# Optimization experiments

Hardware: AMD Instinct MI355X
Metric: run time of the kernel (lower is better)

Reference implementation:

```python
import jax, jax.numpy as jnp
import numpy as np

B, T, D, N = 8, 2048, 1024, 256


def setup_inputs() -> dict:
    key = jax.random.key(0)
    ks = jax.random.split(key, 6)
    sD = 1.0 / np.sqrt(D)
    sN = 1.0 / np.sqrt(N)
    return {
        "x": jax.random.normal(ks[0], (B, T, D), dtype=jnp.float32),
        "Wa": jax.random.normal(ks[1], (D, N), dtype=jnp.float32) * sD,
        "ba": jnp.zeros((N,), jnp.float32),
        "Wb": jax.random.normal(ks[2], (D, N), dtype=jnp.float32) * sD,
        "bb": jnp.zeros((N,), jnp.float32),
        "Wc": jax.random.normal(ks[3], (D, N), dtype=jnp.float32) * sD,
        "bc": jnp.zeros((N,), jnp.float32),
        "Wd": jax.random.normal(ks[4], (D, D), dtype=jnp.float32) * sD,
        "bd": jnp.zeros((D,), jnp.float32),
        "Wy": jax.random.normal(ks[5], (N, D), dtype=jnp.float32) * sN,
        "by": jnp.zeros((D,), jnp.float32),
    }


def reference(x, Wa, ba, Wb, bb, Wc, bc, Wd, bd, Wy, by):
    # Precompute all input-dependent gates/projections in batched GEMMs.
    a = jax.nn.sigmoid(jnp.einsum("btd,dn->btn", x, Wa) + ba)  # (B,T,N)
    b = jnp.einsum("btd,dn->btn", x, Wb) + bb                   # (B,T,N)
    c = jnp.tanh(jnp.einsum("btd,dn->btn", x, Wc) + bc)          # (B,T,N)
    d = jnp.einsum("btd,de->bte", x, Wd) + bd                    # (B,T,D)

    # Sequential linear-gated recurrence: s_t = a_t*s_{t-1} + (1-a_t)*b_t
    def step(s, abc):
        at, bt, ct = abc
        s = at * s + (1.0 - at) * bt
        return s, ct * s

    aT = jnp.swapaxes(a, 0, 1)  # (T,B,N)
    bT = jnp.swapaxes(b, 0, 1)
    cT = jnp.swapaxes(c, 0, 1)
    s0 = jnp.zeros((x.shape[0], Wa.shape[1]), x.dtype)
    _, csT = jax.lax.scan(step, s0, (aT, bT, cT))  # (T,B,N)
    cs = jnp.swapaxes(csT, 0, 1)                    # (B,T,N)

    # Output projection applied once over the full sequence.
    y = jnp.einsum("btn,nd->btd", cs, Wy) + by + d  # (B,T,D)
    return y
```

## Files before the change

### kernel.cpp

```cpp
#include <hip/hip_runtime.h>
#include <hip/hip_bf16.h>

typedef unsigned short u16;
typedef __attribute__((ext_vector_type(8))) short bf16x8;
typedef __attribute__((ext_vector_type(4))) float f32x4;

#define AS1 __attribute__((address_space(1)))
#define AS3 __attribute__((address_space(3)))

#define Bx 8
#define Tt 2048
#define Dd 1024
#define Nn 256
#define Mm (Bx*Tt)
#define CHAINS (Bx*Nn)
#define NCH 32
#define TC 64
#define NCOMB 1792

#define WS_NEED 105644032u

#define CVT_BLOCKS (Mm*Dd/8/256)
#define PACK_BLOCKS (32*32*5)

__device__ __forceinline__ u16 f2bf(float f) {
  union { float f; unsigned u; } v; v.f = f;
  unsigned u = v.u;
  u += 0x7fffu + ((u >> 16) & 1u);
  return (u16)(u >> 16);
}

__device__ __forceinline__ float bf2f(u16 h) {
  union { unsigned u; float f; } v; v.u = ((unsigned)h) << 16;
  return v.f;
}

__device__ __forceinline__ void gload_lds16(const void* g, void* l) {
  __builtin_amdgcn_global_load_lds((AS1 void*)(g), (AS3 void*)(l), 16, 0, 0);
}

__global__ void prep_kernel(const float* __restrict__ x, u16* __restrict__ xb,
                            const float* __restrict__ Wa, const float* __restrict__ Wb,
                            const float* __restrict__ Wc, const float* __restrict__ Wd,
                            const float* __restrict__ Wy,
                            u16* __restrict__ Wcomb, u16* __restrict__ Wyt) {
  const int bid = blockIdx.x;
  if (bid < CVT_BLOCKS) {
    int i = bid * blockDim.x + threadIdx.x;
    #pragma unroll
    for (int j = 0; j < 2; ++j) {
      float4 v = ((const float4*)x)[2*i + j];
      unsigned lo = (unsigned)f2bf(v.x) | ((unsigned)f2bf(v.y) << 16);
      unsigned hi = (unsigned)f2bf(v.z) | ((unsigned)f2bf(v.w) << 16);
      ((uint2*)xb)[2*i + j] = make_uint2(lo, hi);
    }
    return;
  }
  __shared__ float tile[32][33];
  const int pid = bid - CVT_BLOCKS;
  const int z = pid >> 10;
  const int rem = pid & 1023;
  const int bx = rem & 31, by = rem >> 5;
  const float* src; u16* dst; int R, C, dld;
  if (z < 3)       { src = (z==0?Wa:(z==1?Wb:Wc)); dst = Wcomb + (size_t)z*256*1024; R=1024; C=256;  dld=1024; }
  else if (z == 3) { src = Wd; dst = Wcomb + (size_t)768*1024; R=1024; C=1024; dld=1024; }
  else             { src = Wy; dst = Wyt; R=256;  C=1024; dld=256;  }
  int c0 = bx * 32, r0 = by * 32;
  if (c0 >= C || r0 >= R) return;
  int tx = threadIdx.x & 31, ty = threadIdx.x >> 5;
  #pragma unroll
  for (int i = 0; i < 32; i += 8)
    tile[ty + i][tx] = src[(size_t)(r0 + ty + i)*C + (c0 + tx)];
  __syncthreads();
  #pragma unroll
  for (int i = 0; i < 32; i += 8) {
    int c = c0 + ty + i, r = r0 + tx;
    dst[(size_t)c*dld + r] = f2bf(tile[tx][ty + i]);
  }
}

template<int EPI>
__global__ __launch_bounds__(512, 4) void gemm_bt_kernel(
    const u16* __restrict__ A, const u16* __restrict__ Bt, int K, int gx,
    u16* __restrict__ outA, float* __restrict__ outO, u16* __restrict__ dtmp,
    const float* __restrict__ b0, const float* __restrict__ b1,
    const float* __restrict__ b2, const float* __restrict__ b3) {
  __shared__ u16 ldsA[256*64];
  __shared__ u16 ldsB[128*64];
  const int tid = threadIdx.x;
  const int lane = tid & 63, wid = tid >> 6;
  const int wm = wid >> 1, wn = wid & 1;

  const int h = blockIdx.x;
  const int id = (h & 7) * (gridDim.x >> 3) + (h >> 3);
  const int mt = id / gx, nt = id % gx;
  const int m0 = mt * 256, n0 = nt * 128;

  f32x4 acc[4][4] = {};

  const int rl  = tid >> 3;
  const int ssl = (tid & 7) ^ (rl & 7);

  auto stage = [&](int k0) {
    #pragma unroll
    for (int u = 0; u < 4; ++u)
      gload_lds16(A + (size_t)(m0 + u*64 + rl)*K + k0 + ssl*8,
                  ldsA + u*4096 + tid*8);
    #pragma unroll
    for (int u = 0; u < 2; ++u)
      gload_lds16(Bt + (size_t)(n0 + u*64 + rl)*K + k0 + ssl*8,
                  ldsB + u*4096 + tid*8);
  };

  const int lr = lane & 15, kq = lane >> 4, sw = lane & 7;
  const int arow = wm*64 + lr;
  const int brow = wn*64 + lr;

  for (int k0 = 0; k0 < K; k0 += 64) {
    stage(k0);
    __syncthreads();
    #pragma unroll
    for (int kk = 0; kk < 2; ++kk) {
      const int q = ((kk*4 + kq) ^ sw) * 8;
      bf16x8 af[4], bfr[4];
      #pragma unroll
      for (int mi = 0; mi < 4; ++mi)
        af[mi]  = *(const bf16x8*)&ldsA[(arow + mi*16)*64 + q];
      #pragma unroll
      for (int ni = 0; ni < 4; ++ni)
        bfr[ni] = *(const bf16x8*)&ldsB[(brow + ni*16)*64 + q];
      __builtin_amdgcn_s_setprio(1);
      #pragma unroll
      for (int mi = 0; mi < 4; ++mi)
        #pragma unroll
        for (int ni = 0; ni < 4; ++ni)
          acc[mi][ni] = __builtin_amdgcn_mfma_f32_16x16x32_bf16(af[mi], bfr[ni], acc[mi][ni], 0, 0, 0);
      __builtin_amdgcn_s_setprio(0);
    }
    __syncthreads();
  }

  const int crow = m0 + wm*64 + (lane >> 4)*4;
  const int ccol = wn*64 + (lane & 15);
  #pragma unroll
  for (int mi = 0; mi < 4; ++mi) {
    #pragma unroll
    for (int ni = 0; ni < 4; ++ni) {
      int coln = n0 + ccol + ni*16;
      #pragma unroll
      for (int r = 0; r < 4; ++r) {
        int row = crow + mi*16 + r;
        float v = acc[mi][ni][r];
        if (EPI == 0) {
          if (coln < 768) {
            int seg = coln >> 8, cn = coln & 255;
            if (seg == 0)      v = 1.f / (1.f + __expf(-(v + b0[cn])));
            else if (seg == 1) v = v + b1[cn];
            else {
              float e = __expf(2.f*(v + b2[cn]));
              v = 1.f - 2.f/(1.f + e);
            }
            outA[(size_t)row*768 + coln] = f2bf(v);
          } else {
            int col = coln - 768;
            if (dtmp) dtmp[(size_t)row*1024 + col] = f2bf(v + b3[col]);
            else      outO[(size_t)row*1024 + col] = v + b3[col];
          }
        } else {
          const size_t o = (size_t)row*1024 + coln;
          if (dtmp) outO[o] = v + b0[coln] + bf2f(dtmp[o]);
          else      outO[o] = outO[o] + v + b0[coln];
        }
      }
    }
  }
}

__global__ void scanA_kernel(const u16* __restrict__ abc,
                             float* __restrict__ Asum, float* __restrict__ Usum) {
  int idx = blockIdx.x * blockDim.x + threadIdx.x;
  int chain = idx & (CHAINS - 1);
  int ch = idx >> 11;
  int bb = chain >> 8, n = chain & 255;
  const u16* base = abc + (size_t)(bb*Tt + ch*TC) * 768;
  float A = 1.f, U = 0.f;
  for (int t = 0; t < TC; ++t) {
    float a = bf2f(base[(size_t)t*768 + n]);
    float b = bf2f(base[(size_t)t*768 + 256 + n]);
    U = a*U + (1.f - a)*b;
    A *= a;
  }
  Asum[idx] = A; Usum[idx] = U;
}

__global__ void scanB_kernel(const float* __restrict__ Asum, const float* __restrict__ Usum,
                             float* __restrict__ Spre) {
  int chain = blockIdx.x * blockDim.x + threadIdx.x;
  float s = 0.f;
  for (int ch = 0; ch < NCH; ++ch) {
    int i = (ch << 11) + chain;
    Spre[i] = s;
    s = Asum[i]*s + Usum[i];
  }
}

__global__ void scanC_kernel(const u16* __restrict__ abc, const float* __restrict__ Spre,
                             u16* __restrict__ cs) {
  int idx = blockIdx.x * blockDim.x + threadIdx.x;
  int chain = idx & (CHAINS - 1);
  int ch = idx >> 11;
  int bb = chain >> 8, n = chain & 255;
  const u16* base = abc + (size_t)(bb*Tt + ch*TC) * 768;
  u16* csb = cs + (size_t)(bb*Tt + ch*TC) * 256 + n;
  float s = Spre[idx];
  for (int t = 0; t < TC; ++t) {
    float a = bf2f(base[(size_t)t*768 + n]);
    float b = bf2f(base[(size_t)t*768 + 256 + n]);
    float c = bf2f(base[(size_t)t*768 + 512 + n]);
    s = a*s + (1.f - a)*b;
    csb[(size_t)t*256] = f2bf(c*s);
  }
}

extern "C" void kernel_launch(void* const* d_in, const int* in_sizes, int n_in,
                              void* d_out, int out_size, void* d_ws, size_t ws_size,
                              hipStream_t stream) {
  const float* x  = (const float*)d_in[0];
  const float* Wa = (const float*)d_in[1];
  const float* ba = (const float*)d_in[2];
  const float* Wb = (const float*)d_in[3];
  const float* bb = (const float*)d_in[4];
  const float* Wc = (const float*)d_in[5];
  const float* bc = (const float*)d_in[6];
  const float* Wd = (const float*)d_in[7];
  const float* bd = (const float*)d_in[8];
  const float* Wy = (const float*)d_in[9];
  const float* by = (const float*)d_in[10];
  float* out = (float*)d_out;
  char* ws = (char*)d_ws;

  u16*  xb    = (u16*) (ws + 0);
  u16*  Wcomb = (u16*) (ws + 33554432);
  u16*  Wyt   = (u16*) (ws + 37224448);
  u16*  abcb  = (u16*) (ws + 37748736);
  u16*  cs    = (u16*) (ws + 62914560);
  float* Asum = (float*)(ws + 71303168);
  float* Usum = (float*)(ws + 71565312);
  float* Spre = (float*)(ws + 71827456);
  u16*  dtmp  = (ws_size >= WS_NEED) ? (u16*)(ws + 72089600) : nullptr;

  prep_kernel<<<CVT_BLOCKS + PACK_BLOCKS, 256, 0, stream>>>(
      x, xb, Wa, Wb, Wc, Wd, Wy, Wcomb, Wyt);
  gemm_bt_kernel<0><<<896, 512, 0, stream>>>(
      xb, Wcomb, Dd, NCOMB/128, abcb, out, dtmp, ba, bb, bc, bd);
  scanA_kernel<<<CHAINS*NCH/256, 256, 0, stream>>>(abcb, Asum, Usum);
  scanB_kernel<<<CHAINS/256, 256, 0, stream>>>(Asum, Usum, Spre);
  scanC_kernel<<<CHAINS*NCH/256, 256, 0, stream>>>(abcb, Spre, cs);
  gemm_bt_kernel<2><<<512, 512, 0, stream>>>(
      cs, Wyt, Nn, Dd/128, nullptr, out, dtmp, by, nullptr, nullptr, nullptr);
}
```

Before: 150.6 us.

## Double-buffer GEMM K-loop with async LDS prefetch and manual waitcnts

Changes the bf16 GEMM main loop from single-buffered 64-wide K tiles to double-buffered 32-wide tiles. Global-to-LDS loads for tile t+2 are issued while tile t is computed, with explicit vmcnt/lgkmcnt waits, sched barriers and inline-asm ds_read_b128. The goal is to hide global load latency behind MFMA work. In exchange the loop has two barriers per iteration, each step does less MFMA work, and the hand-placed waitcnt ordering is fragile.

```diff
diff --git a/kernel.cpp b/kernel.cpp
--- a/kernel.cpp
+++ b/kernel.cpp
@@ -4,6 +4,7 @@
 typedef unsigned short u16;
 typedef __attribute__((ext_vector_type(8))) short bf16x8;
 typedef __attribute__((ext_vector_type(4))) float f32x4;
+typedef __attribute__((ext_vector_type(4))) int i32x4;
 
 #define AS1 __attribute__((address_space(1)))
 #define AS3 __attribute__((address_space(3)))
@@ -23,6 +24,12 @@
 #define CVT_BLOCKS (Mm*Dd/8/256)
 #define PACK_BLOCKS (32*32*5)
 
+#define VMCNT3 asm volatile("s_waitcnt vmcnt(3)" ::: "memory")
+#define VMCNT0 asm volatile("s_waitcnt vmcnt(0)" ::: "memory")
+#define LGKM0  asm volatile("s_waitcnt lgkmcnt(0)" ::: "memory")
+#define BARR   __builtin_amdgcn_s_barrier()
+#define SCHEDB __builtin_amdgcn_sched_barrier(0)
+
 __device__ __forceinline__ u16 f2bf(float f) {
   union { float f; unsigned u; } v; v.f = f;
   unsigned u = v.u;
@@ -37,6 +44,12 @@
 
 __device__ __forceinline__ void gload_lds16(const void* g, void* l) {
   __builtin_amdgcn_global_load_lds((AS1 void*)(g), (AS3 void*)(l), 16, 0, 0);
+}
+
+__device__ __forceinline__ bf16x8 ds_read_b128_asm(unsigned byte_addr) {
+  i32x4 r;
+  asm volatile("ds_read_b128 %0, %1" : "=v"(r) : "v"(byte_addr));
+  return __builtin_bit_cast(bf16x8, r);
 }
 
 __global__ void prep_kernel(const float* __restrict__ x, u16* __restrict__ xb,
@@ -85,8 +98,8 @@
     u16* __restrict__ outA, float* __restrict__ outO, u16* __restrict__ dtmp,
     const float* __restrict__ b0, const float* __restrict__ b1,
     const float* __restrict__ b2, const float* __restrict__ b3) {
-  __shared__ u16 ldsA[256*64];
-  __shared__ u16 ldsB[128*64];
+  __shared__ u16 ldsA[2*256*32];
+  __shared__ u16 ldsB[2*128*32];
   const int tid = threadIdx.x;
   const int lane = tid & 63, wid = tid >> 6;
   const int wm = wid >> 1, wn = wid & 1;
@@ -95,49 +108,65 @@
   const int id = (h & 7) * (gridDim.x >> 3) + (h >> 3);
   const int mt = id / gx, nt = id % gx;
   const int m0 = mt * 256, n0 = nt * 128;
+  const int NT = K >> 5;
 
   f32x4 acc[4][4] = {};
 
-  const int rl  = tid >> 3;
-  const int ssl = (tid & 7) ^ (rl & 7);
-
-  auto stage = [&](int k0) {
-    #pragma unroll
-    for (int u = 0; u < 4; ++u)
-      gload_lds16(A + (size_t)(m0 + u*64 + rl)*K + k0 + ssl*8,
-                  ldsA + u*4096 + tid*8);
+  const int srow = wid*16 + (lane >> 2);
+  const int sslot = (lane & 3) ^ ((srow >> 1) & 3);
+
+  auto stage = [&](int buf, int t) {
+    const int k0 = t << 5;
     #pragma unroll
     for (int u = 0; u < 2; ++u)
-      gload_lds16(Bt + (size_t)(n0 + u*64 + rl)*K + k0 + ssl*8,
-                  ldsB + u*4096 + tid*8);
+      gload_lds16(A + (size_t)(m0 + u*128 + srow)*K + k0 + sslot*8,
+                  ldsA + buf*8192 + u*4096 + wid*512);
+    gload_lds16(Bt + (size_t)(n0 + srow)*K + k0 + sslot*8,
+                ldsB + buf*4096 + wid*512);
   };
 
-  const int lr = lane & 15, kq = lane >> 4, sw = lane & 7;
-  const int arow = wm*64 + lr;
-  const int brow = wn*64 + lr;
-
-  for (int k0 = 0; k0 < K; k0 += 64) {
-    stage(k0);
-    __syncthreads();
-    #pragma unroll
-    for (int kk = 0; kk < 2; ++kk) {
-      const int q = ((kk*4 + kq) ^ sw) * 8;
-      bf16x8 af[4], bfr[4];
-      #pragma unroll
-      for (int mi = 0; mi < 4; ++mi)
-        af[mi]  = *(const bf16x8*)&ldsA[(arow + mi*16)*64 + q];
+  const int lr = lane & 15, kq = lane >> 4;
+  const int key = (lr >> 1) & 3;
+  const unsigned lbA = (unsigned)(size_t)(AS3 const u16*)ldsA;
+  const unsigned lbB = (unsigned)(size_t)(AS3 const u16*)ldsB;
+  const unsigned aoff = (unsigned)((wm*64 + lr)*64 + ((kq ^ key) << 4));
+  const unsigned boff = (unsigned)((wn*64 + lr)*64 + ((kq ^ key) << 4));
+
+  stage(0, 0);
+  stage(1, (NT > 1) ? 1 : 0);
+  VMCNT3;
+  BARR; SCHEDB;
+
+  for (int t = 0; t < NT; ++t) {
+    const int buf = t & 1;
+    const unsigned ab = lbA + buf*16384 + aoff;
+    const unsigned bb = lbB + buf*8192  + boff;
+
+    bf16x8 af[4], bfr[4];
+    #pragma unroll
+    for (int mi = 0; mi < 4; ++mi) af[mi]  = ds_read_b128_asm(ab + mi*1024);
+    #pragma unroll
+    for (int ni = 0; ni < 4; ++ni) bfr[ni] = ds_read_b128_asm(bb + ni*1024);
+    LGKM0; SCHEDB;
+
+    __builtin_amdgcn_s_setprio(1);
+    #pragma unroll
+    for (int mi = 0; mi < 4; ++mi)
       #pragma unroll
       for (int ni = 0; ni < 4; ++ni)
-        bfr[ni] = *(const bf16x8*)&ldsB[(brow + ni*16)*64 + q];
-      __builtin_amdgcn_s_setprio(1);
-      #pragma unroll
-      for (int mi = 0; mi < 4; ++mi)
-        #pragma unroll
-        for (int ni = 0; ni < 4; ++ni)
-          acc[mi][ni] = __builtin_amdgcn_mfma_f32_16x16x32_bf16(af[mi], bfr[ni], acc[mi][ni], 0, 0, 0);
-      __builtin_amdgcn_s_setprio(0);
+        acc[mi][ni] = __builtin_amdgcn_mfma_f32_16x16x32_bf16(af[mi], bfr[ni], acc[mi][ni], 0, 0, 0);
+    __builtin_amdgcn_s_setprio(0);
+    SCHEDB;
+    BARR; SCHEDB;
+
+    if (t + 2 < NT) {
+      stage(buf, t + 2);
+      VMCNT3;
+    } else {
+      VMCNT0;
     }
-    __syncthreads();
+    SCHEDB;
+    BARR; SCHEDB;
   }
 
   const int crow = m0 + wm*64 + (lane >> 4)*4;
```

Result: slower. 158.9 us (+5.6%).
